# Optimization experiments

Hardware: AMD Instinct MI355X
Metric: run time of the kernel (lower is better)

## Reference

```python
import jax, jax.numpy as jnp
import numpy as np

B, T, C, HEAD = 8, 2048, 1024, 64


def setup_inputs() -> dict:
    key = jax.random.key(0)
    kx, kq, kk, kv = jax.random.split(key, 4)
    x = jax.random.normal(kx, (B, T, C), dtype=jnp.float32)
    Wq = jax.random.normal(kq, (C, HEAD), dtype=jnp.float32) * (C ** -0.5)
    Wk = jax.random.normal(kk, (C, HEAD), dtype=jnp.float32) * (C ** -0.5)
    Wv = jax.random.normal(kv, (C, HEAD), dtype=jnp.float32) * (C ** -0.5)
    return {"x": x, "Wq": Wq, "Wk": Wk, "Wv": Wv}


def reference(x, Wq, Wk, Wv):
    # q,k,v: [B, T, H] via bias-free linear projections
    q = jnp.einsum('btc,ch->bth', x, Wq)
    k = jnp.einsum('btc,ch->bth', x, Wk)
    v = jnp.einsum('btc,ch->bth', x, Wv)
    scale = k.shape[-1] ** -0.5
    # scores: [B, T, T]
    scores = jnp.einsum('bqh,bkh->bqk', q, k) * scale
    Tq = x.shape[1]
    causal = jnp.tril(jnp.ones((Tq, Tq), dtype=bool))  # [T, T]
    scores = jnp.where(causal[None, :, :], scores, -jnp.inf)
    # softmax forced to fp32 in the original (autocast block)
    weight = jax.nn.softmax(scores.astype(jnp.float32), axis=-1)
    # dropout is identity in eval / p=0 deterministic baseline
    out = jnp.einsum('bqk,bkh->bqh', weight.astype(v.dtype), v)  # [B, T, H]
    return out
```

## Files before the change

### kernel.cpp

```cpp
#include <hip/hip_runtime.h>
#include <hip/hip_bf16.h>
#include <stdint.h>

#define NB 8
#define NT 2048
#define NC 1024
#define NH 64

typedef __attribute__((ext_vector_type(8))) short bf16x8;
typedef __attribute__((ext_vector_type(4))) float f32x4;

#define MFMA(a, b, c) __builtin_amdgcn_mfma_f32_16x16x32_bf16((a), (b), (c), 0, 0, 0)

static __device__ __forceinline__ short f2bf(float f) {
  union { float f; uint32_t u; } v; v.f = f;
  uint32_t r = v.u + 0x7FFFu + ((v.u >> 16) & 1u);
  return (short)(r >> 16);
}
static __device__ __forceinline__ float bf2f(short h) {
  union { uint32_t u; float f; } v; v.u = ((uint32_t)(uint16_t)h) << 16;
  return v.f;
}
static __device__ __forceinline__ void gload_lds16(const void* g, void* l) {
  __builtin_amdgcn_global_load_lds(
      (const __attribute__((address_space(1))) uint32_t*)g,
      (__attribute__((address_space(3))) uint32_t*)l, 16, 0, 0);
}

__global__ __launch_bounds__(256) void w_prep(const float* __restrict__ Wq,
                                              const float* __restrict__ Wk,
                                              const float* __restrict__ Wv,
                                              short* __restrict__ Wt) {
  __shared__ short tile[64][68];
  const int blk = blockIdx.x;
  const int mat = blk / 16;
  const int k0 = (blk % 16) * 64;
  const float* W = (mat == 0) ? Wq : (mat == 1) ? Wk : Wv;
  const float scale = (mat == 0) ? 0.125f * 1.44269504088896f : 1.0f;
  const int tid = threadIdx.x;
  {
    int kk = tid >> 2;
    int h0 = (tid & 3) * 16;
    const float* src = W + (size_t)(k0 + kk) * NH + h0;
#pragma unroll
    for (int i = 0; i < 16; ++i) tile[kk][h0 + i] = f2bf(src[i] * scale);
  }
  __syncthreads();
  {
    int j = tid >> 2;
    int kk0 = (tid & 3) * 16;
    bf16x8 t0, t1;
#pragma unroll
    for (int i = 0; i < 8; ++i) { t0[i] = tile[kk0 + i][j]; t1[i] = tile[kk0 + 8 + i][j]; }
    short* dst = Wt + (size_t)(mat * 64 + j) * NC + k0 + kk0;
    *(bf16x8*)dst = t0;
    *(bf16x8*)(dst + 8) = t1;
  }
}

__global__ __launch_bounds__(512) void qkv_proj(const float* __restrict__ x,
                                                const short* __restrict__ Wt,
                                                short* __restrict__ Qo,
                                                short* __restrict__ Ko,
                                                short* __restrict__ VTo) {
  __shared__ char lds_raw[2][32768];
  const int tid = threadIdx.x;
  const int lane = tid & 63;
  const int wave = tid >> 6;
  const int l15 = lane & 15;
  const int hi = lane >> 4;
  const int m0 = blockIdx.x * 32;
  const int wr = wave & 1;
  const int wc = wave >> 1;

  f32x4 acc[3];
#pragma unroll
  for (int f = 0; f < 3; ++f) acc[f] = (f32x4){0.f, 0.f, 0.f, 0.f};

  int xr, xc;
  {
    int off = tid * 16;
    int ol = off ^ (((off >> 8) & 7) << 4);
    xr = ol >> 8; xc = (ol >> 2) & 63;
  }
  int wrow[3], wcol[3];
#pragma unroll
  for (int i = 0; i < 3; ++i) {
    int off = i * 8192 + tid * 16;
    int ol = off ^ (((off >> 7) & 7) << 4);
    wrow[i] = ol >> 7; wcol[i] = (ol >> 1) & 63;
  }

#define STAGE(k0, buf)                                                          \
  {                                                                             \
    char* xsb_ = lds_raw[buf];                                                  \
    char* wtb_ = lds_raw[buf] + 8192;                                           \
    gload_lds16(x + (size_t)(m0 + xr) * NC + (k0) + xc, xsb_ + tid * 16);       \
    _Pragma("unroll")                                                           \
    for (int i = 0; i < 3; ++i)                                                 \
      gload_lds16(Wt + (size_t)wrow[i] * NC + (k0) + wcol[i],                   \
                  wtb_ + i * 8192 + tid * 16);                                  \
  }

  STAGE(0, 0);
  __syncthreads();
  int cur = 0;
  for (int t = 0; t < 16; ++t) {
    if (t + 1 < 16) STAGE((t + 1) * 64, cur ^ 1);
    const char* xsb = lds_raw[cur];
    const char* wtb = lds_raw[cur] + 8192;
    const int r = wr * 16 + l15;
#pragma unroll
    for (int s = 0; s < 2; ++s) {
      int o1 = (r * 256 + s * 128 + hi * 32) ^ ((r & 7) << 4);
      int o2 = (r * 256 + s * 128 + hi * 32 + 16) ^ ((r & 7) << 4);
      float4 q0 = *(const float4*)(xsb + o1);
      float4 q1 = *(const float4*)(xsb + o2);
      bf16x8 a;
      a[0] = f2bf(q0.x); a[1] = f2bf(q0.y); a[2] = f2bf(q0.z); a[3] = f2bf(q0.w);
      a[4] = f2bf(q1.x); a[5] = f2bf(q1.y); a[6] = f2bf(q1.z); a[7] = f2bf(q1.w);
#pragma unroll
      for (int f = 0; f < 3; ++f) {
        int c = wc * 48 + f * 16 + l15;
        int ob = (c * 128 + s * 64 + hi * 16) ^ ((c & 7) << 4);
        bf16x8 b = *(const bf16x8*)(wtb + ob);
        acc[f] = MFMA(a, b, acc[f]);
      }
    }
    __syncthreads();
    cur ^= 1;
  }
#undef STAGE

#pragma unroll
  for (int f = 0; f < 3; ++f) {
    int c = wc * 48 + f * 16 + l15;
    int mat = c >> 6, h = c & 63;
    if (mat < 2) {
      short* dst = (mat == 0) ? Qo : Ko;
#pragma unroll
      for (int r = 0; r < 4; ++r) {
        int t = m0 + wr * 16 + hi * 4 + r;
        dst[(size_t)t * NH + h] = f2bf(acc[f][r]);
      }
    } else {
      int bb = m0 >> 11;
      int t0 = (m0 & 2047) + wr * 16 + hi * 4;
      short4 v;
      v.x = f2bf(acc[f][0]); v.y = f2bf(acc[f][1]);
      v.z = f2bf(acc[f][2]); v.w = f2bf(acc[f][3]);
      *(short4*)(VTo + ((size_t)(bb * 64 + h)) * NT + t0) = v;
    }
  }
}

__global__ __launch_bounds__(256, 2) void attn_fused(const short* __restrict__ Q,
                                                     const short* __restrict__ K,
                                                     const short* __restrict__ Vt,
                                                     float* __restrict__ out) {
  __shared__ short PO[4][32][72];
  __shared__ float Ls[4][32];
  __shared__ short Vs[4][4096];

  const int tid = threadIdx.x;
  const int lane = tid & 63;
  const int wave = tid >> 6;
  const int l15 = lane & 15;
  const int hi = lane >> 4;
  const int kg = hi * 8;

  const int bid = blockIdx.x;
  const int half = bid >> 8;
  const int rr = bid & 255;
  const int b = rr >> 5;
  const int i = rr & 31;
  const int qt = (half == 0) ? (63 - i) : i;
  const int ktmax = qt >> 1;
  const int q0 = qt * 32;

  bf16x8 qf[2][2];
#pragma unroll
  for (int m = 0; m < 2; ++m)
#pragma unroll
    for (int s = 0; s < 2; ++s)
      qf[m][s] = *(const bf16x8*)(Q + ((size_t)b * NT + q0 + m * 16 + l15) * NH +
                                  s * 32 + kg);

  f32x4 oacc[2][4];
#pragma unroll
  for (int m = 0; m < 2; ++m)
#pragma unroll
    for (int f = 0; f < 4; ++f) oacc[m][f] = (f32x4){0.f, 0.f, 0.f, 0.f};
  float ps[2][4];
#pragma unroll
  for (int m = 0; m < 2; ++m)
#pragma unroll
    for (int r = 0; r < 4; ++r) ps[m][r] = 0.f;

#define LOAD_K(dst, kt_)                                                        \
  {                                                                             \
    const short* kb_ = K + ((size_t)b * NT + (kt_) * 64) * NH;                  \
    _Pragma("unroll") for (int n = 0; n < 4; ++n)                               \
    _Pragma("unroll") for (int s = 0; s < 2; ++s)                               \
      dst[n][s] = *(const bf16x8*)(kb_ + (n * 16 + l15) * NH + s * 32 + kg);    \
  }
#define STAGE_V(kt_)                                                            \
  {                                                                             \
    _Pragma("unroll") for (int iv = 0; iv < 8; ++iv) {                          \
      int h_ = iv * 8 + (lane >> 3);                                            \
      int sb_ = (((lane & 7) * 16) ^ ((h_ & 7) << 4)) >> 1;                     \
      gload_lds16(Vt + ((size_t)(b * 64 + h_)) * NT + (kt_) * 64 + sb_,         \
                  &Vs[wave][iv * 512]);                                         \
    }                                                                           \
  }

  int kt = wave;
  bf16x8 kf[4][2];
  if (kt <= ktmax) LOAD_K(kf, kt);

  for (; kt <= ktmax; kt += 4) {
    STAGE_V(kt);

    f32x4 S[2][4];
#pragma unroll
    for (int m = 0; m < 2; ++m)
#pragma unroll
      for (int n = 0; n < 4; ++n) {
        S[m][n] = (f32x4){0.f, 0.f, 0.f, 0.f};
        S[m][n] = MFMA(qf[m][0], kf[n][0], S[m][n]);
        S[m][n] = MFMA(qf[m][1], kf[n][1], S[m][n]);
      }

    bf16x8 kn[4][2];
    const bool more = (kt + 4) <= ktmax;
    if (more) LOAD_K(kn, kt + 4);

    if (kt == ktmax) {
#pragma unroll
      for (int m = 0; m < 2; ++m)
#pragma unroll
        for (int n = 0; n < 4; ++n)
#pragma unroll
          for (int r = 0; r < 4; ++r)
            if (kt * 64 + n * 16 + l15 > q0 + m * 16 + hi * 4 + r)
              S[m][n][r] = -INFINITY;
    }
#pragma unroll
    for (int m = 0; m < 2; ++m)
#pragma unroll
      for (int n = 0; n < 4; ++n)
#pragma unroll
        for (int r = 0; r < 4; ++r) {
          float p = __builtin_amdgcn_exp2f(S[m][n][r]);
          S[m][n][r] = p;
          ps[m][r] += p;
        }

#pragma unroll
    for (int m = 0; m < 2; ++m)
#pragma unroll
      for (int n = 0; n < 4; ++n)
#pragma unroll
        for (int r = 0; r < 4; ++r)
          PO[wave][m * 16 + hi * 4 + r][n * 16 + l15] = f2bf(S[m][n][r]);

    bf16x8 pa[2][2];
#pragma unroll
    for (int m = 0; m < 2; ++m)
#pragma unroll
      for (int s = 0; s < 2; ++s)
        pa[m][s] = *(const bf16x8*)&PO[wave][m * 16 + l15][s * 32 + kg];

    asm volatile("s_waitcnt vmcnt(0)" ::: "memory");
    __builtin_amdgcn_sched_barrier(0);

    bf16x8 vf[4][2];
#pragma unroll
    for (int f = 0; f < 4; ++f)
#pragma unroll
      for (int s = 0; s < 2; ++s) {
        int h_ = f * 16 + l15;
        int ob = h_ * 128 + (((s * 32 + kg) * 2) ^ ((h_ & 7) << 4));
        vf[f][s] = *(const bf16x8*)((const char*)&Vs[wave][0] + ob);
      }
#pragma unroll
    for (int m = 0; m < 2; ++m)
#pragma unroll
      for (int f = 0; f < 4; ++f) {
        oacc[m][f] = MFMA(pa[m][0], vf[f][0], oacc[m][f]);
        oacc[m][f] = MFMA(pa[m][1], vf[f][1], oacc[m][f]);
      }
    if (more) {
#pragma unroll
      for (int n = 0; n < 4; ++n)
#pragma unroll
        for (int s = 0; s < 2; ++s) kf[n][s] = kn[n][s];
    }
  }
#undef LOAD_K
#undef STAGE_V

#pragma unroll
  for (int d = 1; d < 16; d <<= 1)
#pragma unroll
    for (int m = 0; m < 2; ++m)
#pragma unroll
      for (int r = 0; r < 4; ++r) ps[m][r] += __shfl_xor(ps[m][r], d);

  if (l15 == 0) {
#pragma unroll
    for (int m = 0; m < 2; ++m)
#pragma unroll
      for (int r = 0; r < 4; ++r)
        Ls[wave][m * 16 + hi * 4 + r] = ps[m][r];
  }
#pragma unroll
  for (int m = 0; m < 2; ++m)
#pragma unroll
    for (int f = 0; f < 4; ++f)
#pragma unroll
      for (int r = 0; r < 4; ++r)
        PO[wave][m * 16 + hi * 4 + r][f * 16 + l15] = f2bf(oacc[m][f][r]);
  __syncthreads();

  {
    const int row = tid >> 3;
    const int c0 = (tid & 7) * 8;
    float L = 0.f;
    float o[8] = {0.f, 0.f, 0.f, 0.f, 0.f, 0.f, 0.f, 0.f};
#pragma unroll
    for (int w = 0; w < 4; ++w) {
      L += Ls[w][row];
      short4 v0 = *(const short4*)&PO[w][row][c0];
      short4 v1 = *(const short4*)&PO[w][row][c0 + 4];
      o[0] += bf2f(v0.x); o[1] += bf2f(v0.y); o[2] += bf2f(v0.z); o[3] += bf2f(v0.w);
      o[4] += bf2f(v1.x); o[5] += bf2f(v1.y); o[6] += bf2f(v1.z); o[7] += bf2f(v1.w);
    }
    float inv = 1.f / L;
    float* po = out + ((size_t)b * NT + q0 + row) * NH + c0;
    float4 r0 = {o[0] * inv, o[1] * inv, o[2] * inv, o[3] * inv};
    float4 r1 = {o[4] * inv, o[5] * inv, o[6] * inv, o[7] * inv};
    *(float4*)po = r0;
    *(float4*)(po + 4) = r1;
  }
}

extern "C" void kernel_launch(void* const* d_in, const int* in_sizes, int n_in,
                              void* d_out, int out_size, void* d_ws, size_t ws_size,
                              hipStream_t stream) {
  const float* x  = (const float*)d_in[0];
  const float* Wq = (const float*)d_in[1];
  const float* Wk = (const float*)d_in[2];
  const float* Wv = (const float*)d_in[3];
  float* out = (float*)d_out;

  char* ws = (char*)d_ws;
  short* Wt = (short*)ws;
  short* Qb = (short*)(ws + (size_t)(1 << 20));
  short* Kb = (short*)(ws + (size_t)(3 << 20));
  short* Vt = (short*)(ws + (size_t)(5 << 20));

  hipLaunchKernelGGL(w_prep, dim3(48), dim3(256), 0, stream, Wq, Wk, Wv, Wt);
  hipLaunchKernelGGL(qkv_proj, dim3(512), dim3(512), 0, stream, x, Wt, Qb, Kb, Vt);
  hipLaunchKernelGGL(attn_fused, dim3(512), dim3(256), 0, stream, Qb, Kb, Vt, out);
}
```

Measured before the change: 45.25 us.

## Stage K tiles through LDS with async loads and prefetch next K/V tiles

K tiles are now loaded asynchronously into a per-wave swizzled LDS buffer via global_load_lds instead of into registers. The next K and V tiles are issued one iteration ahead, using vmcnt-counted waits so global latency overlaps with MFMA and softmax work. This frees the registers that held the prefetched K fragments and drops the min-blocks launch hint. In exchange it adds 32 KB of LDS per block, which may reduce occupancy, and it relies on fragile hand-written waitcnt ordering.

Result: slower. 52.43 us (+15.9%).

```diff
diff --git a/kernel.cpp b/kernel.cpp
--- a/kernel.cpp
+++ b/kernel.cpp
@@ -154,12 +154,13 @@
   }
 }
 
-__global__ __launch_bounds__(256, 2) void attn_fused(const short* __restrict__ Q,
-                                                     const short* __restrict__ K,
-                                                     const short* __restrict__ Vt,
-                                                     float* __restrict__ out) {
+__global__ __launch_bounds__(256) void attn_fused(const short* __restrict__ Q,
+                                                  const short* __restrict__ K,
+                                                  const short* __restrict__ Vt,
+                                                  float* __restrict__ out) {
   __shared__ short PO[4][32][72];
   __shared__ float Ls[4][32];
+  __shared__ short Ks[4][4096];
   __shared__ short Vs[4][4096];
 
   const int tid = threadIdx.x;
@@ -197,29 +198,47 @@
 #pragma unroll
     for (int r = 0; r < 4; ++r) ps[m][r] = 0.f;
 
-#define LOAD_K(dst, kt_)                                                        \
+#define ISSUE_K(kt_)                                                            \
   {                                                                             \
-    const short* kb_ = K + ((size_t)b * NT + (kt_) * 64) * NH;                  \
-    _Pragma("unroll") for (int n = 0; n < 4; ++n)                               \
-    _Pragma("unroll") for (int s = 0; s < 2; ++s)                               \
-      dst[n][s] = *(const bf16x8*)(kb_ + (n * 16 + l15) * NH + s * 32 + kg);    \
-  }
-#define STAGE_V(kt_)                                                            \
+    _Pragma("unroll") for (int iv = 0; iv < 8; ++iv) {                          \
+      int r_ = iv * 8 + (lane >> 3);                                            \
+      int c_ = (lane & 7) ^ (r_ & 7);                                           \
+      gload_lds16(K + ((size_t)b * NT + (kt_) * 64 + r_) * NH + c_ * 8,         \
+                  &Ks[wave][iv * 512]);                                         \
+    }                                                                           \
+  }
+#define ISSUE_V(kt_)                                                            \
   {                                                                             \
     _Pragma("unroll") for (int iv = 0; iv < 8; ++iv) {                          \
       int h_ = iv * 8 + (lane >> 3);                                            \
-      int sb_ = (((lane & 7) * 16) ^ ((h_ & 7) << 4)) >> 1;                     \
-      gload_lds16(Vt + ((size_t)(b * 64 + h_)) * NT + (kt_) * 64 + sb_,         \
+      int c_ = (lane & 7) ^ (h_ & 7);                                           \
+      gload_lds16(Vt + ((size_t)(b * 64 + h_)) * NT + (kt_) * 64 + c_ * 8,      \
                   &Vs[wave][iv * 512]);                                         \
     }                                                                           \
   }
 
   int kt = wave;
-  bf16x8 kf[4][2];
-  if (kt <= ktmax) LOAD_K(kf, kt);
+  if (kt <= ktmax) { ISSUE_K(kt); ISSUE_V(kt); }
 
   for (; kt <= ktmax; kt += 4) {
-    STAGE_V(kt);
+    const bool more = (kt + 4) <= ktmax;
+
+    asm volatile("s_waitcnt vmcnt(8)" ::: "memory");
+    __builtin_amdgcn_sched_barrier(0);
+    bf16x8 kf[4][2];
+#pragma unroll
+    for (int n = 0; n < 4; ++n)
+#pragma unroll
+      for (int s = 0; s < 2; ++s) {
+        int r_ = n * 16 + l15;
+        int c_ = (s * 4 + hi) ^ (r_ & 7);
+        kf[n][s] = *(const bf16x8*)((const char*)&Ks[wave][0] + r_ * 128 + c_ * 16);
+      }
+    if (more) {
+      asm volatile("s_waitcnt lgkmcnt(0)" ::: "memory");
+      __builtin_amdgcn_sched_barrier(0);
+      ISSUE_K(kt + 4);
+    }
 
     f32x4 S[2][4];
 #pragma unroll
@@ -230,11 +249,6 @@
         S[m][n] = MFMA(qf[m][0], kf[n][0], S[m][n]);
         S[m][n] = MFMA(qf[m][1], kf[n][1], S[m][n]);
       }
-
-    bf16x8 kn[4][2];
-    const bool more = (kt + 4) <= ktmax;
-    if (more) LOAD_K(kn, kt + 4);
-
     if (kt == ktmax) {
 #pragma unroll
       for (int m = 0; m < 2; ++m)
@@ -271,18 +285,23 @@
       for (int s = 0; s < 2; ++s)
         pa[m][s] = *(const bf16x8*)&PO[wave][m * 16 + l15][s * 32 + kg];
 
-    asm volatile("s_waitcnt vmcnt(0)" ::: "memory");
+    if (more) asm volatile("s_waitcnt vmcnt(8)" ::: "memory");
+    else      asm volatile("s_waitcnt vmcnt(0)" ::: "memory");
     __builtin_amdgcn_sched_barrier(0);
-
     bf16x8 vf[4][2];
 #pragma unroll
     for (int f = 0; f < 4; ++f)
 #pragma unroll
       for (int s = 0; s < 2; ++s) {
         int h_ = f * 16 + l15;
-        int ob = h_ * 128 + (((s * 32 + kg) * 2) ^ ((h_ & 7) << 4));
+        int ob = h_ * 128 + (((s * 4 + hi) ^ (h_ & 7)) * 16);
         vf[f][s] = *(const bf16x8*)((const char*)&Vs[wave][0] + ob);
       }
+    if (more) {
+      asm volatile("s_waitcnt lgkmcnt(0)" ::: "memory");
+      __builtin_amdgcn_sched_barrier(0);
+      ISSUE_V(kt + 4);
+    }
 #pragma unroll
     for (int m = 0; m < 2; ++m)
 #pragma unroll
@@ -290,15 +309,9 @@
         oacc[m][f] = MFMA(pa[m][0], vf[f][0], oacc[m][f]);
         oacc[m][f] = MFMA(pa[m][1], vf[f][1], oacc[m][f]);
       }
-    if (more) {
-#pragma unroll
-      for (int n = 0; n < 4; ++n)
-#pragma unroll
-        for (int s = 0; s < 2; ++s) kf[n][s] = kn[n][s];
-    }
-  }
-#undef LOAD_K
-#undef STAGE_V
+  }
+#undef ISSUE_K
+#undef ISSUE_V
 
 #pragma unroll
   for (int d = 1; d < 16; d <<= 1)
```
